# Kernel tuning notes

Hardware: AMD Instinct MI355X
Metric: run time of the kernel (lower is better)

Reference implementation:

```python
import jax, jax.numpy as jnp
import numpy as np

B, LQ, LK = 64, 128, 1024
E, H = 768, 6
HD = E // H            # 128
D2 = HD // 2           # 64
LNUM = 2
QD, KD = 768, 768
EPS = 1e-5


def _gn(x, g, b):
    # torch.nn.GroupNorm(H, E) on 2D input [N, E]: normalize per group of HD channels
    N = x.shape[0]
    xg = x.reshape(N, H, HD)
    m = xg.mean(-1, keepdims=True)
    v = xg.var(-1, keepdims=True)
    xn = ((xg - m) / jnp.sqrt(v + EPS)).reshape(N, E)
    return xn * g + b


def _ln(x, g, b):
    m = x.mean(-1, keepdims=True)
    v = x.var(-1, keepdims=True)
    return (x - m) / jnp.sqrt(v + EPS) * g + b


def setup_inputs() -> dict:
    key = jax.random.key(0)
    ks = iter(jax.random.split(key, 64))
    def rn(shape, s=0.02):
        return jax.random.normal(next(ks), shape, dtype=jnp.float32) * s
    L = LNUM
    inp = {}
    inp['q_feat'] = jax.random.normal(next(ks), (B, LQ, QD), dtype=jnp.float32)
    inp['k_feats'] = jax.random.normal(next(ks), (B, LK, KD), dtype=jnp.float32)
    inp['q_mask'] = jnp.ones((B, LQ), jnp.float32)
    inp['k_mask'] = jnp.ones((B, LK), jnp.float32)
    # per-layer projections (stacked along layer axis)
    inp['Wq'] = rn((L, QD, E)); inp['bq'] = jnp.zeros((L, E)); inp['gq_g'] = jnp.ones((L, E)); inp['gq_b'] = jnp.zeros((L, E))
    inp['Wk'] = rn((L, KD, E)); inp['bk'] = jnp.zeros((L, E)); inp['gk_g'] = jnp.ones((L, E)); inp['gk_b'] = jnp.zeros((L, E))
    inp['Wv1'] = rn((L, QD, E)); inp['bv1'] = jnp.zeros((L, E)); inp['g1_g'] = jnp.ones((L, E)); inp['g1_b'] = jnp.zeros((L, E))
    inp['Wv2'] = rn((L, KD, E)); inp['bv2'] = jnp.zeros((L, E)); inp['g2_g'] = jnp.ones((L, E)); inp['g2_b'] = jnp.zeros((L, E))
    # inner Attention net (per layer)
    inp['Wab'] = rn((L, HD, D2)); inp['bab'] = jnp.zeros((L, D2))
    inp['Wal'] = rn((L, D2, 1)); inp['bal'] = jnp.zeros((L, 1))
    inp['Wac'] = rn((L, D2, HD)); inp['bac'] = jnp.zeros((L, HD))
    # bifeat_emb + layer norms (layer_num-1 of them)
    inp['Wbi'] = rn((L - 1, 2 * E, E)); inp['bbi'] = jnp.zeros((L - 1, E))
    inp['lnb_g'] = jnp.ones((L - 1, E)); inp['lnb_b'] = jnp.zeros((L - 1, E))
    # final proj + layernorm
    inp['Wp'] = rn((E * L + QD, E)); inp['bp'] = jnp.zeros((E,))
    inp['ln_g'] = jnp.ones((E,)); inp['ln_b'] = jnp.zeros((E,))
    return inp


def _bilinear_attention(q, k, kmask, p):
    (Wq, bq, gqg, gqb, Wk, bk, gkg, gkb, Wv1, bv1, g1g, g1b,
     Wv2, bv2, g2g, g2b, Wab, bab, Wal, bal, Wac, bac) = p
    Bb = q.shape[0]
    Lk = k.shape[1]
    qp = _gn(jnp.tanh(q @ Wq + bq), gqg, gqb).reshape(Bb, H, HD)      # [B,H,HD]
    v1 = _gn(jnp.tanh(q @ Wv1 + bv1), g1g, g1b).reshape(Bb, H, HD)
    kf = k.reshape(-1, k.shape[-1])
    kp = _gn(jnp.tanh(kf @ Wk + bk), gkg, gkb).reshape(Bb, Lk, H, HD).transpose(0, 2, 1, 3)   # [B,H,Lk,HD]
    v2 = _gn(jnp.tanh(kf @ Wv2 + bv2), g2g, g2b).reshape(Bb, Lk, H, HD).transpose(0, 2, 1, 3)
    att_map = qp[:, :, None, :] * kp                                  # [B,H,Lk,HD] bilinear map
    basic = jax.nn.relu(att_map @ Wab + bab)                          # [B,H,Lk,D2]
    mext = kmask[:, None, :, None]                                    # [B,1,Lk,1]
    pool = (basic * mext).sum(2) / mext.sum(2)                        # masked mean -> [B,H,D2]
    a_s = (basic @ Wal + bal)[..., 0]                                 # [B,H,Lk]
    a_s = jnp.where(kmask[:, None, :] == 0, -1e9, a_s)
    a_s = jax.nn.softmax(a_s, axis=-1)
    a_c = jax.nn.sigmoid(pool @ Wac + bac)                            # [B,H,HD] channel gate
    v2a = jnp.einsum('bhl,bhld->bhd', a_s, v2)
    return (v1 * v2a * a_c).reshape(Bb, E)


def reference(q_feat, k_feats, q_mask, k_mask,
              Wq, bq, gq_g, gq_b, Wk, bk, gk_g, gk_b,
              Wv1, bv1, g1_g, g1_b, Wv2, bv2, g2_g, g2_b,
              Wab, bab, Wal, bal, Wac, bac,
              Wbi, bbi, lnb_g, lnb_b, Wp, bp, ln_g, ln_b):
    qm = q_mask[..., None]
    q = (q_feat * qm).sum(1) / qm.sum(1)                              # masked mean pool -> [B,QD]
    feats = [q]
    k = k_feats
    for i in range(LNUM):
        p = (Wq[i], bq[i], gq_g[i], gq_b[i], Wk[i], bk[i], gk_g[i], gk_b[i],
             Wv1[i], bv1[i], g1_g[i], g1_b[i], Wv2[i], bv2[i], g2_g[i], g2_b[i],
             Wab[i], bab[i], Wal[i], bal[i], Wac[i], bac[i])
        q = _bilinear_attention(q, k, k_mask, p)                      # dropout = identity (eval)
        feats.append(q)
        if i < LNUM - 1:
            cat = jnp.concatenate([jnp.broadcast_to(q[:, None, :], k.shape), k], axis=-1)
            k = _ln(jax.nn.relu(cat @ Wbi[i] + bbi[i]) + k, lnb_g[i], lnb_b[i])
    out = _ln(jnp.concatenate(feats, axis=-1) @ Wp + bp, ln_g, ln_b)
    return out
```

## Files before the change

kernel.cpp:

```cpp
#include <hip/hip_runtime.h>
#include <math.h>

#define DEVI static __device__ __forceinline__

typedef unsigned short u16;
typedef __attribute__((ext_vector_type(8))) short short8;
typedef __attribute__((ext_vector_type(4))) float f32x4;

DEVI float bf2f(u16 u) { union { float f; unsigned int i; } c; c.i = ((unsigned int)u) << 16; return c.f; }
DEVI u16 f2bf(float f) {
  union { float f; unsigned int i; } c; c.f = f;
  unsigned int r = c.i + 0x7FFFu + ((c.i >> 16) & 1u);
  return (u16)(r >> 16);
}

DEVI float ftanh(float x) {
  float e = __expf(2.f * x);
  return 1.f - 2.f * __builtin_amdgcn_rcpf(e + 1.f);
}

DEVI void gld16(const u16* g, u16* l) {
  __builtin_amdgcn_global_load_lds((const __attribute__((address_space(1))) unsigned int*)g,
                                   (__attribute__((address_space(3))) unsigned int*)l, 16, 0, 0);
}

#define BB 64
#define LQN 128
#define LKN 1024
#define EN 768
#define HN 6
#define HDN 128
#define D2N 64
#define EPSV 1e-5f

__global__ __launch_bounds__(256) void transpose_w5(
    const float* __restrict__ Wk, const float* __restrict__ Wv2,
    const float* __restrict__ Wbi, u16* __restrict__ WkvT,
    u16* __restrict__ WbiT) {
  __shared__ float tile[32][33];
  int z = blockIdx.z;
  const float* src;
  u16* dst;
  if (z < 2) { src = Wk + (size_t)z * EN * EN; dst = WkvT + (size_t)z * 1536 * EN; }
  else if (z < 4) { src = Wv2 + (size_t)(z - 2) * EN * EN; dst = WkvT + (size_t)(z - 2) * 1536 * EN + (size_t)EN * EN; }
  else { src = Wbi + (size_t)EN * EN; dst = WbiT; }
  int kb = blockIdx.x * 32, nb = blockIdx.y * 32;
  int tx = threadIdx.x, ty = threadIdx.y;
  for (int j = 0; j < 32; j += 8)
    tile[ty + j][tx] = src[(size_t)(kb + ty + j) * EN + nb + tx];
  __syncthreads();
  for (int j = 0; j < 32; j += 8)
    dst[(size_t)(nb + ty + j) * EN + kb + tx] = f2bf(tile[tx][ty + j]);
}

__global__ __launch_bounds__(256) void transpose_cvt(
    const float* __restrict__ src, u16* __restrict__ dst, int K, int N,
    size_t srcZ, size_t dstZ) {
  __shared__ float tile[32][33];
  src += (size_t)blockIdx.z * srcZ;
  dst += (size_t)blockIdx.z * dstZ;
  int kb = blockIdx.x * 32, nb = blockIdx.y * 32;
  int tx = threadIdx.x, ty = threadIdx.y;
  for (int j = 0; j < 32; j += 8)
    tile[ty + j][tx] = src[(size_t)(kb + ty + j) * N + nb + tx];
  __syncthreads();
  for (int j = 0; j < 32; j += 8)
    dst[(size_t)(nb + ty + j) * K + kb + tx] = f2bf(tile[tx][ty + j]);
}

__global__ void conv_bf16(const float* __restrict__ src, u16* __restrict__ dst, size_t n8) {
  size_t i = (size_t)blockIdx.x * 256 + threadIdx.x;
  if (i >= n8) return;
  float4 a = ((const float4*)src)[2 * i];
  float4 b = ((const float4*)src)[2 * i + 1];
  short8 o;
  o[0] = (short)f2bf(a.x); o[1] = (short)f2bf(a.y); o[2] = (short)f2bf(a.z); o[3] = (short)f2bf(a.w);
  o[4] = (short)f2bf(b.x); o[5] = (short)f2bf(b.y); o[6] = (short)f2bf(b.z); o[7] = (short)f2bf(b.w);
  *(short8*)&dst[i * 8] = o;
}

__global__ __launch_bounds__(768) void poolq_kernel(
    const float* __restrict__ qf, const float* __restrict__ qm,
    float* __restrict__ q_cur, float* __restrict__ feats) {
  int t = threadIdx.x, b = blockIdx.x;
  float s = 0.f, ms = 0.f;
  for (int l = 0; l < LQN; ++l) {
    float w = qm[b * LQN + l];
    s += qf[((size_t)b * LQN + l) * EN + t] * w;
    ms += w;
  }
  float q = s / ms;
  q_cur[(size_t)b * EN + t] = q;
  feats[(size_t)b * 3 * EN + t] = q;
}

__global__ __launch_bounds__(256) void msum_kernel(const float* __restrict__ km, float* __restrict__ msum) {
  __shared__ float red[256];
  int t = threadIdx.x, b = blockIdx.x;
  float s = 0.f;
  for (int l = t; l < LKN; l += 256) s += km[b * LKN + l];
  red[t] = s; __syncthreads();
  for (int o = 128; o > 0; o >>= 1) { if (t < o) red[t] += red[t + o]; __syncthreads(); }
  if (t == 0) msum[b] = red[0];
}

__global__ __launch_bounds__(768) void qside2_kernel(
    const float* __restrict__ q_in,
    const float* __restrict__ W0, const float* __restrict__ b0,
    const float* __restrict__ g0, const float* __restrict__ bb0, float* __restrict__ o0,
    const float* __restrict__ W1, const float* __restrict__ b1,
    const float* __restrict__ g1, const float* __restrict__ bb1, float* __restrict__ o1,
    const float* __restrict__ W2, const float* __restrict__ b2, float* __restrict__ o2) {
  __shared__ float qs[EN];
  __shared__ float ys[EN];
  __shared__ float mh[HN], rh[HN];
  int t = threadIdx.x, b = blockIdx.x, which = blockIdx.y;
  const float* W = which == 0 ? W0 : (which == 1 ? W1 : W2);
  const float* bvec = which == 0 ? b0 : (which == 1 ? b1 : b2);
  qs[t] = q_in[(size_t)b * EN + t];
  __syncthreads();
  float acc = 0.f;
  for (int k = 0; k < EN; ++k) acc += qs[k] * W[(size_t)k * EN + t];
  if (which == 2) {
    o2[(size_t)b * EN + t] = acc + bvec[t];
    return;
  }
  const float* g = which ? g1 : g0;
  const float* bb = which ? bb1 : bb0;
  float* outp = which ? o1 : o0;
  float y = tanhf(acc + bvec[t]);
  ys[t] = y; __syncthreads();
  if (t < HN) {
    float s = 0.f, s2 = 0.f;
    for (int d = 0; d < HDN; ++d) { float v = ys[t * HDN + d]; s += v; s2 += v * v; }
    float m = s * (1.f / HDN), var = s2 * (1.f / HDN) - m * m;
    mh[t] = m; rh[t] = rsqrtf(var + EPSV);
  }
  __syncthreads();
  int h = t >> 7;
  outp[(size_t)b * EN + t] = (y - mh[h]) * rh[h] * g[t] + bb[t];
}

__global__ __launch_bounds__(256, 4) void gemm_proj(
    const u16* __restrict__ A, const u16* __restrict__ BT,
    const float* __restrict__ bias_k, const float* __restrict__ g_k,
    const float* __restrict__ bb_k, const float* __restrict__ qp,
    const float* __restrict__ bias_v, const float* __restrict__ g_v,
    const float* __restrict__ bb_v, u16* __restrict__ out_v,
    const u16* __restrict__ Wab_g, const float* __restrict__ bab_g,
    const float* __restrict__ Wal_g, const float* __restrict__ bal_g,
    const float* __restrict__ kmask, float* __restrict__ s_out,
    float* __restrict__ pool_part) {
  const int K = EN;
  __shared__ __align__(16) u16 SM[16384];
  __shared__ float part2[128][2][2];
  __shared__ float pool_sh[4][64];
  u16* As = SM;
  u16* Bs = SM + 8192;
  int t = threadIdx.x;
  int w = t >> 6, lane = t & 63;
  int wm = w >> 1, wn = w & 1;

  int bid = blockIdx.x;
  int swz = ((bid & 7) * 768) + (bid >> 3);
  int rowT = swz / 12, cT = swz % 12;
  int rowBase = rowT << 7;

  int koff = (((lane & 3) ^ ((lane >> 3) & 3)) << 3);
  const u16* gA = A + (size_t)(rowBase + (w << 5) + (lane >> 2)) * K + koff;
  const u16* gB = BT + (size_t)((cT << 7) + (w << 5) + (lane >> 2)) * K + koff;

  int lrow = lane & 15, kq = lane >> 4;
  int sOff = ((kq ^ ((lrow >> 1) & 3)) << 3);
  f32x4 acc[4][4] = {};

  u16* lA0b = As + (w << 10);
  u16* lB0b = Bs + (w << 10);
  u16* lA1b = As + 4096 + (w << 10);
  u16* lB1b = Bs + 4096 + (w << 10);

#define PROJ_PREF(LA, LB, k0) \
    { gld16(gA + (k0), LA); gld16(gA + (size_t)16 * K + (k0), LA + 512); \
      gld16(gB + (k0), LB); gld16(gB + (size_t)16 * K + (k0), LB + 512); }

#define PROJ_STEP(BASE) \
    { short8 af[4], bf[4]; \
      _Pragma("unroll") \
      for (int m = 0; m < 4; ++m) \
        af[m] = *(const short8*)&As[(BASE) + ((wm * 64 + m * 16 + lrow) << 5) + sOff]; \
      _Pragma("unroll") \
      for (int n = 0; n < 4; ++n) \
        bf[n] = *(const short8*)&Bs[(BASE) + ((wn * 64 + n * 16 + lrow) << 5) + sOff]; \
      _Pragma("unroll") \
      for (int m = 0; m < 4; ++m) \
        _Pragma("unroll") \
        for (int n = 0; n < 4; ++n) \
          acc[m][n] = __builtin_amdgcn_mfma_f32_16x16x32_bf16(af[m], bf[n], acc[m][n], 0, 0, 0); }

  PROJ_PREF(lA0b, lB0b, 0)
#pragma unroll 1
  for (int p = 0; p < 12; ++p) {
    __syncthreads();
    PROJ_PREF(lA1b, lB1b, (2 * p + 1) << 5)
    PROJ_STEP(0)
    __syncthreads();
    if (p < 11) PROJ_PREF(lA0b, lB0b, (2 * p + 2) << 5)
    PROJ_STEP(4096)
  }
#undef PROJ_PREF
#undef PROJ_STEP

  __syncthreads();

  const int which = cT >= 6;
  const int ecol = ((which ? cT - 6 : cT) << 7);
  const float* bias = which ? bias_v : bias_k;
  const int bidx = rowBase >> 10;

  {
    float biasv[4];
#pragma unroll
    for (int n = 0; n < 4; ++n)
      biasv[n] = bias[ecol + wn * 64 + n * 16 + lrow];
#pragma unroll
    for (int m = 0; m < 4; ++m)
#pragma unroll
      for (int j = 0; j < 4; ++j) {
        int row = wm * 64 + m * 16 + kq * 4 + j;
#pragma unroll
        for (int n = 0; n < 4; ++n) {
          float y = ftanh(acc[m][n][j] + biasv[n]);
          int c = wn * 64 + n * 16 + lrow;
          int sl = c >> 3;
          int so = ((sl & 7) ^ (row & 7)) | (sl & 8);
          SM[row * 128 + (so << 3) + (c & 7)] = f2bf(y);
        }
      }
  }
  __syncthreads();

  {
    int row = t >> 1, ch = t & 1;
    short8 yv8[8];
    float s = 0.f, s2 = 0.f;
#pragma unroll
    for (int s8 = 0; s8 < 8; ++s8) {
      int sl = (ch << 3) + s8;
      int so = ((sl & 7) ^ (row & 7)) | (sl & 8);
      yv8[s8] = *(const short8*)&SM[row * 128 + (so << 3)];
#pragma unroll
      for (int i = 0; i < 8; ++i) {
        float y = bf2f((u16)yv8[s8][i]);
        s += y; s2 += y * y;
      }
    }
    part2[row][ch][0] = s; part2[row][ch][1] = s2;
    __syncthreads();
    float ssum = part2[row][0][0] + part2[row][1][0];
    float q2 = part2[row][0][1] + part2[row][1][1];
    float mean = ssum * (1.f / 128.f);
    float var = q2 * (1.f / 128.f) - mean * mean;
    float rstd = rsqrtf(var + EPSV);
    const float* gp = which ? g_v : g_k;
    const float* bbp = which ? bb_v : bb_k;
    size_t R = (size_t)rowBase + row;
#pragma unroll
    for (int s8 = 0; s8 < 8; ++s8) {
      int sl = (ch << 3) + s8;
      int so = ((sl & 7) ^ (row & 7)) | (sl & 8);
      int e0 = ecol + (sl << 3);
      float4 g0 = *(const float4*)&gp[e0];
      float4 g1 = *(const float4*)&gp[e0 + 4];
      float4 b0 = *(const float4*)&bbp[e0];
      float4 b1 = *(const float4*)&bbp[e0 + 4];
      float gg[8] = {g0.x, g0.y, g0.z, g0.w, g1.x, g1.y, g1.z, g1.w};
      float bv8[8] = {b0.x, b0.y, b0.z, b0.w, b1.x, b1.y, b1.z, b1.w};
      float ov[8];
#pragma unroll
      for (int i = 0; i < 8; ++i)
        ov[i] = (bf2f((u16)yv8[s8][i]) - mean) * rstd * gg[i] + bv8[i];
      if (!which) {
        float4 q0 = *(const float4*)&qp[(size_t)bidx * EN + e0];
        float4 q1 = *(const float4*)&qp[(size_t)bidx * EN + e0 + 4];
        float qq[8] = {q0.x, q0.y, q0.z, q0.w, q1.x, q1.y, q1.z, q1.w};
#pragma unroll
        for (int i = 0; i < 8; ++i) ov[i] *= qq[i];
      }
      short8 o8;
#pragma unroll
      for (int i = 0; i < 8; ++i) o8[i] = (short)f2bf(ov[i]);
      if (which) *(short8*)&out_v[R * EN + e0] = o8;
      else       *(short8*)&SM[row * 128 + (so << 3)] = o8;
    }
  }
  if (which) return;
  __syncthreads();

  const int h = cT;
  const int lt = (rowBase >> 7) & 7;
  f32x4 acc2[2][4] = {};
#pragma unroll
  for (int ks = 0; ks < 4; ++ks) {
    short8 af2[2], bf2[4];
#pragma unroll
    for (int mm = 0; mm < 2; ++mm) {
      int l = w * 32 + mm * 16 + lrow;
      int sl = ks * 4 + kq;
      int so = ((sl & 7) ^ (l & 7)) | (sl & 8);
      af2[mm] = *(const short8*)&SM[l * 128 + so * 8];
    }
#pragma unroll
    for (int n = 0; n < 4; ++n)
      bf2[n] = *(const short8*)&Wab_g[(size_t)(n * 16 + lrow) * 128 + ks * 32 + kq * 8];
#pragma unroll
    for (int mm = 0; mm < 2; ++mm)
#pragma unroll
      for (int n = 0; n < 4; ++n)
        acc2[mm][n] = __builtin_amdgcn_mfma_f32_16x16x32_bf16(af2[mm], bf2[n], acc2[mm][n], 0, 0, 0);
  }

  float wv[4], bv[4];
#pragma unroll
  for (int n = 0; n < 4; ++n) { int c = n * 16 + lrow; wv[n] = Wal_g[c]; bv[n] = bab_g[c]; }
  float kmv[2][4];
  const float* km = kmask + (size_t)bidx * LKN + lt * 128;
#pragma unroll
  for (int mm = 0; mm < 2; ++mm)
#pragma unroll
    for (int j = 0; j < 4; ++j) kmv[mm][j] = km[w * 32 + mm * 16 + kq * 4 + j];
  float balv = bal_g[0];
  float pp[4] = {0.f, 0.f, 0.f, 0.f};
#pragma unroll
  for (int mm = 0; mm < 2; ++mm)
#pragma unroll
    for (int j = 0; j < 4; ++j) {
      float sp = 0.f;
#pragma unroll
      for (int n = 0; n < 4; ++n) {
        float bsv = fmaxf(acc2[mm][n][j] + bv[n], 0.f);
        sp += bsv * wv[n];
        pp[n] += bsv * kmv[mm][j];
      }
      sp += __shfl_xor(sp, 1, 64);
      sp += __shfl_xor(sp, 2, 64);
      sp += __shfl_xor(sp, 4, 64);
      sp += __shfl_xor(sp, 8, 64);
      if (lrow == 0)
        s_out[(((size_t)bidx * HN + h) << 10) + lt * 128 + w * 32 + mm * 16 + kq * 4 + j] = sp + balv;
    }
#pragma unroll
  for (int n = 0; n < 4; ++n) {
    pp[n] += __shfl_xor(pp[n], 16, 64);
    pp[n] += __shfl_xor(pp[n], 32, 64);
  }
  if (lane < 16) {
#pragma unroll
    for (int n = 0; n < 4; ++n) pool_sh[w][n * 16 + lane] = pp[n];
  }
  __syncthreads();
  if (t < 64) {
    float p = pool_sh[0][t] + pool_sh[1][t] + pool_sh[2][t] + pool_sh[3][t];
    pool_part[((((size_t)bidx * HN + h) << 3) + lt) * 64 + t] = p;
  }
}

__global__ __launch_bounds__(256, 4) void gemm_bilin(
    const u16* __restrict__ A, const u16* __restrict__ BT,
    const float* __restrict__ biasB, const u16* __restrict__ resid,
    u16* __restrict__ out) {
  const int K = EN;
  __shared__ __align__(16) u16 SM[16384];
  u16* As = SM;
  u16* Bs = SM + 8192;
  int t = threadIdx.x;
  int w = t >> 6, lane = t & 63;
  int wm = w >> 1, wn = w & 1;

  int bid = blockIdx.x;
  int swz = ((bid & 7) * 384) + (bid >> 3);
  int rowT = swz / 6, cT = swz % 6;
  int rowBase = rowT << 7;
  int colBase = cT << 7;

  int koff = (((lane & 3) ^ ((lane >> 3) & 3)) << 3);
  const u16* gA = A + (size_t)(rowBase + (w << 5) + (lane >> 2)) * K + koff;
  const u16* gB = BT + (size_t)(colBase + (w << 5) + (lane >> 2)) * K + koff;

  int lrow = lane & 15, kq = lane >> 4;
  int sOff = ((kq ^ ((lrow >> 1) & 3)) << 3);
  f32x4 acc[4][4] = {};

  u16* lA0b = As + (w << 10);
  u16* lB0b = Bs + (w << 10);
  u16* lA1b = As + 4096 + (w << 10);
  u16* lB1b = Bs + 4096 + (w << 10);

#define BIL_PREF(LA, LB, k0) \
    { gld16(gA + (k0), LA); gld16(gA + (size_t)16 * K + (k0), LA + 512); \
      gld16(gB + (k0), LB); gld16(gB + (size_t)16 * K + (k0), LB + 512); }

#define BIL_STEP(BASE) \
    { short8 af[4], bf[4]; \
      _Pragma("unroll") \
      for (int m = 0; m < 4; ++m) \
        af[m] = *(const short8*)&As[(BASE) + ((wm * 64 + m * 16 + lrow) << 5) + sOff]; \
      _Pragma("unroll") \
      for (int n = 0; n < 4; ++n) \
        bf[n] = *(const short8*)&Bs[(BASE) + ((wn * 64 + n * 16 + lrow) << 5) + sOff]; \
      _Pragma("unroll") \
      for (int m = 0; m < 4; ++m) \
        _Pragma("unroll") \
        for (int n = 0; n < 4; ++n) \
          acc[m][n] = __builtin_amdgcn_mfma_f32_16x16x32_bf16(af[m], bf[n], acc[m][n], 0, 0, 0); }

  BIL_PREF(lA0b, lB0b, 0)
#pragma unroll 1
  for (int p = 0; p < 12; ++p) {
    __syncthreads();
    BIL_PREF(lA1b, lB1b, (2 * p + 1) << 5)
    BIL_STEP(0)
    __syncthreads();
    if (p < 11) BIL_PREF(lA0b, lB0b, (2 * p + 2) << 5)
    BIL_STEP(4096)
  }
#undef BIL_PREF
#undef BIL_STEP

  __syncthreads();

  const int bidx = rowBase >> 10;
  {
    float qv[4];
#pragma unroll
    for (int n = 0; n < 4; ++n)
      qv[n] = biasB[(size_t)bidx * EN + colBase + wn * 64 + n * 16 + lrow];
#pragma unroll
    for (int m = 0; m < 4; ++m)
#pragma unroll
      for (int j = 0; j < 4; ++j) {
        int row = wm * 64 + m * 16 + kq * 4 + j;
#pragma unroll
        for (int n = 0; n < 4; ++n) {
          float y = fmaxf(acc[m][n][j] + qv[n], 0.f);
          int c = wn * 64 + n * 16 + lrow;
          int sl = c >> 3;
          int so = ((sl & 7) ^ (row & 7)) | (sl & 8);
          SM[row * 128 + (so << 3) + (c & 7)] = f2bf(y);
        }
      }
  }
  __syncthreads();

  {
    int row = t >> 1, ch = t & 1;
    size_t R = (size_t)rowBase + row;
#pragma unroll
    for (int s8 = 0; s8 < 8; ++s8) {
      int sl = (ch << 3) + s8;
      int so = ((sl & 7) ^ (row & 7)) | (sl & 8);
      short8 yv = *(const short8*)&SM[row * 128 + (so << 3)];
      int e0 = colBase + (sl << 3);
      short8 rv = *(const short8*)&resid[R * EN + e0];
      short8 o8;
#pragma unroll
      for (int i = 0; i < 8; ++i)
        o8[i] = (short)f2bf(bf2f((u16)yv[i]) + bf2f((u16)rv[i]));
      *(short8*)&out[R * EN + e0] = o8;
    }
  }
}

__global__ __launch_bounds__(256) void attn_fin(
    const float* __restrict__ s_in, const float* __restrict__ kmask,
    const float* __restrict__ msum, const float* __restrict__ pool_part,
    const float* __restrict__ Wac, const float* __restrict__ bac,
    const u16* __restrict__ v2, const float* __restrict__ v1,
    float* __restrict__ q_cur, float* __restrict__ feats, int slot) {
  __shared__ float as_sh[LKN];
  __shared__ float red[256];
  __shared__ float red8[16][129];
  __shared__ float pool_sh[64];
  __shared__ float ac_sh[128];
  int t = threadIdx.x;
  int h = blockIdx.x, b = blockIdx.y;
  const float* sb = s_in + (((size_t)b * HN + h) << 10);
  const float* km = kmask + (size_t)b * LKN;
  float v[4];
  float mx = -1e30f;
#pragma unroll
  for (int j = 0; j < 4; ++j) {
    int l = t * 4 + j;
    float x = sb[l];
    if (km[l] == 0.f) x = -1e9f;
    v[j] = x; mx = fmaxf(mx, x);
  }
  red[t] = mx; __syncthreads();
  for (int o = 128; o > 0; o >>= 1) { if (t < o) red[t] = fmaxf(red[t], red[t + o]); __syncthreads(); }
  float mxv = red[0];
  __syncthreads();
  float sum = 0.f;
#pragma unroll
  for (int j = 0; j < 4; ++j) { v[j] = __expf(v[j] - mxv); sum += v[j]; }
  red[t] = sum; __syncthreads();
  for (int o = 128; o > 0; o >>= 1) { if (t < o) red[t] += red[t + o]; __syncthreads(); }
  float inv = 1.f / red[0];
#pragma unroll
  for (int j = 0; j < 4; ++j) as_sh[t * 4 + j] = v[j] * inv;
  if (t < 64) {
    float p = 0.f;
    for (int lt = 0; lt < 8; ++lt)
      p += pool_part[((((size_t)b * HN + h) << 3) + lt) * 64 + t];
    pool_sh[t] = p / msum[b];
  }
  __syncthreads();
  if (t < 128) {
    float a = 0.f;
    for (int j = 0; j < 64; ++j) a += pool_sh[j] * Wac[j * HDN + t];
    ac_sh[t] = 1.f / (1.f + __expf(-(a + bac[t])));
  }
  __syncthreads();
  {
    int o = t & 15, sl = t >> 4;
    const u16* vb = v2 + ((size_t)b * LKN) * EN + h * HDN + o * 8;
    float a8[8] = {};
    for (int l = sl; l < LKN; l += 16) {
      short8 u = *(const short8*)&vb[(size_t)l * EN];
      float wgt = as_sh[l];
#pragma unroll
      for (int i = 0; i < 8; ++i) a8[i] += wgt * bf2f((u16)u[i]);
    }
#pragma unroll
    for (int i = 0; i < 8; ++i) red8[sl][o * 8 + i] = a8[i];
  }
  __syncthreads();
  if (t < 128) {
    float va = 0.f;
#pragma unroll
    for (int s = 0; s < 16; ++s) va += red8[s][t];
    size_t idx = (size_t)b * EN + h * HDN + t;
    float q = v1[idx] * va * ac_sh[t];
    q_cur[idx] = q;
    feats[(size_t)b * 3 * EN + slot * EN + h * HDN + t] = q;
  }
}

__global__ __launch_bounds__(256) void ln_rows_kernel(
    const u16* __restrict__ z, const float* __restrict__ g,
    const float* __restrict__ bb, u16* __restrict__ outp) {
  int t = threadIdx.x, w = t >> 6, lane = t & 63;
  size_t R = (size_t)blockIdx.x * 4 + w;
  const u16* zr = z + R * EN;
  float xv[12];
  float s = 0.f, s2 = 0.f;
#pragma unroll
  for (int c = 0; c < 3; ++c) {
    ushort4 u = *(const ushort4*)&zr[c * 256 + lane * 4];
    float v0 = bf2f(u.x), v1 = bf2f(u.y), v2 = bf2f(u.z), v3 = bf2f(u.w);
    xv[c * 4 + 0] = v0; xv[c * 4 + 1] = v1; xv[c * 4 + 2] = v2; xv[c * 4 + 3] = v3;
    s += v0 + v1 + v2 + v3;
    s2 += v0 * v0 + v1 * v1 + v2 * v2 + v3 * v3;
  }
#pragma unroll
  for (int o = 1; o < 64; o <<= 1) { s += __shfl_xor(s, o, 64); s2 += __shfl_xor(s2, o, 64); }
  float m = s * (1.f / EN), var = s2 * (1.f / EN) - m * m;
  float r = rsqrtf(var + EPSV);
#pragma unroll
  for (int c = 0; c < 3; ++c) {
    ushort4 o4;
    int e = c * 256 + lane * 4;
    o4.x = f2bf((xv[c * 4 + 0] - m) * r * g[e + 0] + bb[e + 0]);
    o4.y = f2bf((xv[c * 4 + 1] - m) * r * g[e + 1] + bb[e + 1]);
    o4.z = f2bf((xv[c * 4 + 2] - m) * r * g[e + 2] + bb[e + 2]);
    o4.w = f2bf((xv[c * 4 + 3] - m) * r * g[e + 3] + bb[e + 3]);
    *(ushort4*)&outp[R * EN + e] = o4;
  }
}

__global__ __launch_bounds__(768) void final_kernel(
    const float* __restrict__ feats, const float* __restrict__ Wp,
    const float* __restrict__ bp, const float* __restrict__ g,
    const float* __restrict__ bb, float* __restrict__ outp) {
  __shared__ float fs[2304];
  __shared__ float red[24];
  __shared__ float mv[2];
  int t = threadIdx.x, b = blockIdx.x;
  fs[t] = feats[(size_t)b * 2304 + t];
  fs[t + 768] = feats[(size_t)b * 2304 + 768 + t];
  fs[t + 1536] = feats[(size_t)b * 2304 + 1536 + t];
  __syncthreads();
  float acc = 0.f;
  for (int k = 0; k < 2304; ++k) acc += fs[k] * Wp[(size_t)k * EN + t];
  float y = acc + bp[t];
  float s = y, s2 = y * y;
  for (int o = 32; o > 0; o >>= 1) { s += __shfl_down(s, o, 64); s2 += __shfl_down(s2, o, 64); }
  int wid = t >> 6, lane = t & 63;
  if (lane == 0) { red[wid] = s; red[12 + wid] = s2; }
  __syncthreads();
  if (t == 0) {
    float ts = 0.f, ts2 = 0.f;
    for (int i = 0; i < 12; ++i) { ts += red[i]; ts2 += red[12 + i]; }
    float m = ts * (1.f / EN), var = ts2 * (1.f / EN) - m * m;
    mv[0] = m; mv[1] = rsqrtf(var + EPSV);
  }
  __syncthreads();
  outp[(size_t)b * EN + t] = (y - mv[0]) * mv[1] * g[t] + bb[t];
}

extern "C" void kernel_launch(void* const* d_in, const int* in_sizes, int n_in,
                              void* d_out, int out_size, void* d_ws, size_t ws_size,
                              hipStream_t stream) {
  const float* q_feat = (const float*)d_in[0];
  const float* k_feats = (const float*)d_in[1];
  const float* q_mask = (const float*)d_in[2];
  const float* k_mask = (const float*)d_in[3];
  const float* Wq = (const float*)d_in[4];
  const float* bq = (const float*)d_in[5];
  const float* gq_g = (const float*)d_in[6];
  const float* gq_b = (const float*)d_in[7];
  const float* Wk = (const float*)d_in[8];
  const float* bk = (const float*)d_in[9];
  const float* gk_g = (const float*)d_in[10];
  const float* gk_b = (const float*)d_in[11];
  const float* Wv1 = (const float*)d_in[12];
  const float* bv1 = (const float*)d_in[13];
  const float* g1_g = (const float*)d_in[14];
  const float* g1_b = (const float*)d_in[15];
  const float* Wv2 = (const float*)d_in[16];
  const float* bv2 = (const float*)d_in[17];
  const float* g2_g = (const float*)d_in[18];
  const float* g2_b = (const float*)d_in[19];
  const float* Wab = (const float*)d_in[20];
  const float* bab = (const float*)d_in[21];
  const float* Wal = (const float*)d_in[22];
  const float* bal = (const float*)d_in[23];
  const float* Wac = (const float*)d_in[24];
  const float* bac = (const float*)d_in[25];
  const float* Wbi = (const float*)d_in[26];
  const float* bbi = (const float*)d_in[27];
  const float* lnb_g = (const float*)d_in[28];
  const float* lnb_b = (const float*)d_in[29];
  const float* Wp = (const float*)d_in[30];
  const float* bp = (const float*)d_in[31];
  const float* ln_g = (const float*)d_in[32];
  const float* ln_b = (const float*)d_in[33];
  float* out = (float*)d_out;
  (void)in_sizes; (void)n_in; (void)out_size; (void)ws_size;

  char* ws = (char*)d_ws;
  size_t off = 0;
  auto alloc = [&](size_t bytes) -> char* {
    char* p = ws + off;
    off += (bytes + 255) & ~(size_t)255;
    return p;
  };
  const size_t MK = (size_t)BB * LKN;
  u16* kf = (u16*)alloc(MK * EN * 2);
  u16* zbuf = (u16*)alloc(MK * EN * 2);
  u16* v2b = (u16*)alloc(MK * EN * 2);
  u16* WkvT = (u16*)alloc((size_t)2 * 1536 * EN * 2);
  u16* WbiT = (u16*)alloc((size_t)EN * EN * 2);
  u16* WabT = (u16*)alloc((size_t)2 * D2N * HDN * 2);
  float* feats = (float*)alloc((size_t)BB * 3 * EN * 4);
  float* q_cur = (float*)alloc((size_t)BB * EN * 4);
  float* qp = (float*)alloc((size_t)BB * EN * 4);
  float* v1 = (float*)alloc((size_t)BB * EN * 4);
  float* qpart = (float*)alloc((size_t)BB * EN * 4);
  float* sbuf = (float*)alloc((size_t)BB * HN * LKN * 4);
  float* poolp = (float*)alloc((size_t)BB * HN * 8 * D2N * 4);
  float* msum = (float*)alloc((size_t)BB * 4);

  dim3 tb(32, 8);
  transpose_w5<<<dim3(24, 24, 5), tb, 0, stream>>>(Wk, Wv2, Wbi, WkvT, WbiT);
  transpose_cvt<<<dim3(4, 2, 2), tb, 0, stream>>>(Wab, WabT, HDN, D2N, (size_t)HDN * D2N, (size_t)D2N * HDN);

  conv_bf16<<<24576, 256, 0, stream>>>(k_feats, kf, MK * EN / 8);
  poolq_kernel<<<BB, EN, 0, stream>>>(q_feat, q_mask, q_cur, feats);
  msum_kernel<<<BB, 256, 0, stream>>>(k_mask, msum);

  qside2_kernel<<<dim3(BB, 2), 768, 0, stream>>>(
      q_cur, Wq, bq, gq_g, gq_b, qp,
      Wv1, bv1, g1_g, g1_b, v1, nullptr, nullptr, nullptr);
  gemm_proj<<<6144, 256, 0, stream>>>(
      kf, WkvT, bk, gk_g, gk_b, qp,
      bv2, g2_g, g2_b, v2b,
      WabT, bab, Wal, bal, k_mask, sbuf, poolp);
  attn_fin<<<dim3(HN, BB), 256, 0, stream>>>(
      sbuf, k_mask, msum, poolp, Wac, bac, v2b, v1, q_cur, feats, 1);

  qside2_kernel<<<dim3(BB, 3), 768, 0, stream>>>(
      q_cur, Wq + (size_t)EN * EN, bq + EN, gq_g + EN, gq_b + EN, qp,
      Wv1 + (size_t)EN * EN, bv1 + EN, g1_g + EN, g1_b + EN, v1,
      Wbi, bbi, qpart);
  gemm_bilin<<<3072, 256, 0, stream>>>(kf, WbiT, qpart, kf, zbuf);
  ln_rows_kernel<<<MK / 4, 256, 0, stream>>>(zbuf, lnb_g, lnb_b, kf);
  gemm_proj<<<6144, 256, 0, stream>>>(
      kf, WkvT + (size_t)1536 * EN, bk + EN, gk_g + EN, gk_b + EN, qp,
      bv2 + EN, g2_g + EN, g2_b + EN, v2b,
      WabT + (size_t)D2N * HDN, bab + D2N, Wal + D2N, bal + 1, k_mask, sbuf, poolp);
  attn_fin<<<dim3(HN, BB), 256, 0, stream>>>(
      sbuf, k_mask, msum, poolp, Wac + (size_t)D2N * HDN, bac + HDN, v2b, v1, q_cur, feats, 2);

  final_kernel<<<BB, EN, 0, stream>>>(feats, Wp, bp, ln_g, ln_b, out);
}
```

Before: 971.7 us.

## Fold layer-norm into the next projection GEMM via row stats and weight scaling

The separate LayerNorm pass over the 64K x 768 intermediate is removed. Per-row partial sums are accumulated in the bilinear GEMM epilogue, finished by a small stats kernel, and the LN gain is folded into the layer-2 K/V2 weights. The mean and bias terms are applied as a rank-1 correction (rstd*acc - m*rstd*u + vb) in the projection epilogue. This saves a full read and write of the large activation, at the cost of feeding the GEMM unnormalized bf16 inputs, which can lose precision when row means are large.

```diff
diff --git a/kernel.cpp b/kernel.cpp
--- a/kernel.cpp
+++ b/kernel.cpp
@@ -35,19 +35,23 @@
 
 __global__ __launch_bounds__(256) void transpose_w5(
     const float* __restrict__ Wk, const float* __restrict__ Wv2,
-    const float* __restrict__ Wbi, u16* __restrict__ WkvT,
-    u16* __restrict__ WbiT) {
+    const float* __restrict__ Wbi, const float* __restrict__ lnb_g,
+    u16* __restrict__ WkvT, u16* __restrict__ WbiT) {
   __shared__ float tile[32][33];
   int z = blockIdx.z;
   const float* src;
   u16* dst;
+  bool fold = (z == 1) || (z == 3);
   if (z < 2) { src = Wk + (size_t)z * EN * EN; dst = WkvT + (size_t)z * 1536 * EN; }
   else if (z < 4) { src = Wv2 + (size_t)(z - 2) * EN * EN; dst = WkvT + (size_t)(z - 2) * 1536 * EN + (size_t)EN * EN; }
   else { src = Wbi + (size_t)EN * EN; dst = WbiT; }
   int kb = blockIdx.x * 32, nb = blockIdx.y * 32;
   int tx = threadIdx.x, ty = threadIdx.y;
-  for (int j = 0; j < 32; j += 8)
-    tile[ty + j][tx] = src[(size_t)(kb + ty + j) * EN + nb + tx];
+  for (int j = 0; j < 32; j += 8) {
+    float v = src[(size_t)(kb + ty + j) * EN + nb + tx];
+    if (fold) v *= lnb_g[kb + ty + j];
+    tile[ty + j][tx] = v;
+  }
   __syncthreads();
   for (int j = 0; j < 32; j += 8)
     dst[(size_t)(nb + ty + j) * EN + kb + tx] = f2bf(tile[tx][ty + j]);
@@ -66,6 +70,41 @@
   __syncthreads();
   for (int j = 0; j < 32; j += 8)
     dst[(size_t)(nb + ty + j) * K + kb + tx] = f2bf(tile[tx][ty + j]);
+}
+
+__global__ __launch_bounds__(256) void uv_kernel(
+    const float* __restrict__ WkL1, const float* __restrict__ Wv2L1,
+    const float* __restrict__ g, const float* __restrict__ bbv,
+    const float* __restrict__ bkL1, const float* __restrict__ bv2L1,
+    float* __restrict__ uvec, float* __restrict__ vbvec) {
+  int c = blockIdx.x * 256 + threadIdx.x;
+  int part = c >= EN;
+  int cc = part ? c - EN : c;
+  const float* W = part ? Wv2L1 : WkL1;
+  float u = 0.f, vb = 0.f;
+  for (int k = 0; k < EN; ++k) {
+    float w = W[(size_t)k * EN + cc];
+    u += g[k] * w;
+    vb += bbv[k] * w;
+  }
+  vb += part ? bv2L1[cc] : bkL1[cc];
+  uvec[c] = u;
+  vbvec[c] = vb;
+}
+
+__global__ __launch_bounds__(256) void finstat_kernel(
+    const float2* __restrict__ rowpart, float2* __restrict__ rowstat) {
+  int R = blockIdx.x * 256 + threadIdx.x;
+  float s = 0.f, s2 = 0.f;
+#pragma unroll
+  for (int i = 0; i < 6; ++i) {
+    float2 p = rowpart[(size_t)i * (BB * LKN) + R];
+    s += p.x; s2 += p.y;
+  }
+  float m = s * (1.f / EN);
+  float var = s2 * (1.f / EN) - m * m;
+  float rstd = rsqrtf(var + EPSV);
+  rowstat[R] = make_float2(rstd, -m * rstd);
 }
 
 __global__ void conv_bf16(const float* __restrict__ src, u16* __restrict__ dst, size_t n8) {
@@ -150,7 +189,9 @@
     const u16* __restrict__ Wab_g, const float* __restrict__ bab_g,
     const float* __restrict__ Wal_g, const float* __restrict__ bal_g,
     const float* __restrict__ kmask, float* __restrict__ s_out,
-    float* __restrict__ pool_part) {
+    float* __restrict__ pool_part,
+    const float2* __restrict__ rowstat, const float* __restrict__ uvec,
+    const float* __restrict__ vbvec) {
   const int K = EN;
   __shared__ __align__(16) u16 SM[16384];
   __shared__ float part2[128][2][2];
@@ -218,18 +259,33 @@
   const int bidx = rowBase >> 10;
 
   {
-    float biasv[4];
-#pragma unroll
-    for (int n = 0; n < 4; ++n)
-      biasv[n] = bias[ecol + wn * 64 + n * 16 + lrow];
+    float biasv[4], un[4], vbn[4];
+    if (rowstat) {
+#pragma unroll
+      for (int n = 0; n < 4; ++n) {
+        int cc = (cT << 7) + wn * 64 + n * 16 + lrow;
+        un[n] = uvec[cc]; vbn[n] = vbvec[cc];
+      }
+    } else {
+#pragma unroll
+      for (int n = 0; n < 4; ++n)
+        biasv[n] = bias[ecol + wn * 64 + n * 16 + lrow];
+    }
 #pragma unroll
     for (int m = 0; m < 4; ++m)
 #pragma unroll
       for (int j = 0; j < 4; ++j) {
         int row = wm * 64 + m * 16 + kq * 4 + j;
+        float rstd = 1.f, m2 = 0.f;
+        if (rowstat) {
+          float2 st = rowstat[rowBase + row];
+          rstd = st.x; m2 = st.y;
+        }
 #pragma unroll
         for (int n = 0; n < 4; ++n) {
-          float y = ftanh(acc[m][n][j] + biasv[n]);
+          float pre = rowstat ? (rstd * acc[m][n][j] + m2 * un[n] + vbn[n])
+                              : (acc[m][n][j] + biasv[n]);
+          float y = ftanh(pre);
           int c = wn * 64 + n * 16 + lrow;
           int sl = c >> 3;
           int so = ((sl & 7) ^ (row & 7)) | (sl & 8);
@@ -367,9 +423,10 @@
 __global__ __launch_bounds__(256, 4) void gemm_bilin(
     const u16* __restrict__ A, const u16* __restrict__ BT,
     const float* __restrict__ biasB, const u16* __restrict__ resid,
-    u16* __restrict__ out) {
+    u16* __restrict__ out, float2* __restrict__ rowpart) {
   const int K = EN;
   __shared__ __align__(16) u16 SM[16384];
+  __shared__ float bps[128], bpq[128];
   u16* As = SM;
   u16* Bs = SM + 8192;
   int t = threadIdx.x;
@@ -454,6 +511,7 @@
   {
     int row = t >> 1, ch = t & 1;
     size_t R = (size_t)rowBase + row;
+    float s = 0.f, s2 = 0.f;
 #pragma unroll
     for (int s8 = 0; s8 < 8; ++s8) {
       int sl = (ch << 3) + s8;
@@ -463,10 +521,18 @@
       short8 rv = *(const short8*)&resid[R * EN + e0];
       short8 o8;
 #pragma unroll
-      for (int i = 0; i < 8; ++i)
-        o8[i] = (short)f2bf(bf2f((u16)yv[i]) + bf2f((u16)rv[i]));
+      for (int i = 0; i < 8; ++i) {
+        u16 zb = f2bf(bf2f((u16)yv[i]) + bf2f((u16)rv[i]));
+        o8[i] = (short)zb;
+        float zf = bf2f(zb);
+        s += zf; s2 += zf * zf;
+      }
       *(short8*)&out[R * EN + e0] = o8;
     }
+    if (ch == 1) { bps[row] = s; bpq[row] = s2; }
+    __syncthreads();
+    if (ch == 0)
+      rowpart[(size_t)cT * (BB * LKN) + R] = make_float2(s + bps[row], s2 + bpq[row]);
   }
 }
 
@@ -541,38 +607,6 @@
     float q = v1[idx] * va * ac_sh[t];
     q_cur[idx] = q;
     feats[(size_t)b * 3 * EN + slot * EN + h * HDN + t] = q;
-  }
-}
-
-__global__ __launch_bounds__(256) void ln_rows_kernel(
-    const u16* __restrict__ z, const float* __restrict__ g,
-    const float* __restrict__ bb, u16* __restrict__ outp) {
-  int t = threadIdx.x, w = t >> 6, lane = t & 63;
-  size_t R = (size_t)blockIdx.x * 4 + w;
-  const u16* zr = z + R * EN;
-  float xv[12];
-  float s = 0.f, s2 = 0.f;
-#pragma unroll
-  for (int c = 0; c < 3; ++c) {
-    ushort4 u = *(const ushort4*)&zr[c * 256 + lane * 4];
-    float v0 = bf2f(u.x), v1 = bf2f(u.y), v2 = bf2f(u.z), v3 = bf2f(u.w);
-    xv[c * 4 + 0] = v0; xv[c * 4 + 1] = v1; xv[c * 4 + 2] = v2; xv[c * 4 + 3] = v3;
-    s += v0 + v1 + v2 + v3;
-    s2 += v0 * v0 + v1 * v1 + v2 * v2 + v3 * v3;
-  }
-#pragma unroll
-  for (int o = 1; o < 64; o <<= 1) { s += __shfl_xor(s, o, 64); s2 += __shfl_xor(s2, o, 64); }
-  float m = s * (1.f / EN), var = s2 * (1.f / EN) - m * m;
-  float r = rsqrtf(var + EPSV);
-#pragma unroll
-  for (int c = 0; c < 3; ++c) {
-    ushort4 o4;
-    int e = c * 256 + lane * 4;
-    o4.x = f2bf((xv[c * 4 + 0] - m) * r * g[e + 0] + bb[e + 0]);
-    o4.y = f2bf((xv[c * 4 + 1] - m) * r * g[e + 1] + bb[e + 1]);
-    o4.z = f2bf((xv[c * 4 + 2] - m) * r * g[e + 2] + bb[e + 2]);
-    o4.w = f2bf((xv[c * 4 + 3] - m) * r * g[e + 3] + bb[e + 3]);
-    *(ushort4*)&outp[R * EN + e] = o4;
   }
 }
 
@@ -668,10 +702,16 @@
   float* sbuf = (float*)alloc((size_t)BB * HN * LKN * 4);
   float* poolp = (float*)alloc((size_t)BB * HN * 8 * D2N * 4);
   float* msum = (float*)alloc((size_t)BB * 4);
+  float2* rowpart = (float2*)alloc((size_t)6 * MK * 8);
+  float2* rowstat = (float2*)alloc(MK * 8);
+  float* uvec = (float*)alloc(1536 * 4);
+  float* vbvec = (float*)alloc(1536 * 4);
 
   dim3 tb(32, 8);
-  transpose_w5<<<dim3(24, 24, 5), tb, 0, stream>>>(Wk, Wv2, Wbi, WkvT, WbiT);
+  transpose_w5<<<dim3(24, 24, 5), tb, 0, stream>>>(Wk, Wv2, Wbi, lnb_g, WkvT, WbiT);
   transpose_cvt<<<dim3(4, 2, 2), tb, 0, stream>>>(Wab, WabT, HDN, D2N, (size_t)HDN * D2N, (size_t)D2N * HDN);
+  uv_kernel<<<6, 256, 0, stream>>>(Wk + (size_t)EN * EN, Wv2 + (size_t)EN * EN,
+                                   lnb_g, lnb_b, bk + EN, bv2 + EN, uvec, vbvec);
 
   conv_bf16<<<24576, 256, 0, stream>>>(k_feats, kf, MK * EN / 8);
   poolq_kernel<<<BB, EN, 0, stream>>>(q_feat, q_mask, q_cur, feats);
@@ -683,7 +723,8 @@
   gemm_proj<<<6144, 256, 0, stream>>>(
       kf, WkvT, bk, gk_g, gk_b, qp,
       bv2, g2_g, g2_b, v2b,
-      WabT, bab, Wal, bal, k_mask, sbuf, poolp);
+      WabT, bab, Wal, bal, k_mask, sbuf, poolp,
+      nullptr, nullptr, nullptr);
   attn_fin<<<dim3(HN, BB), 256, 0, stream>>>(
       sbuf, k_mask, msum, poolp, Wac, bac, v2b, v1, q_cur, feats, 1);
 
@@ -691,12 +732,13 @@
       q_cur, Wq + (size_t)EN * EN, bq + EN, gq_g + EN, gq_b + EN, qp,
       Wv1 + (size_t)EN * EN, bv1 + EN, g1_g + EN, g1_b + EN, v1,
       Wbi, bbi, qpart);
-  gemm_bilin<<<3072, 256, 0, stream>>>(kf, WbiT, qpart, kf, zbuf);
-  ln_rows_kernel<<<MK / 4, 256, 0, stream>>>(zbuf, lnb_g, lnb_b, kf);
+  gemm_bilin<<<3072, 256, 0, stream>>>(kf, WbiT, qpart, kf, zbuf, rowpart);
+  finstat_kernel<<<MK / 256, 256, 0, stream>>>(rowpart, rowstat);
   gemm_proj<<<6144, 256, 0, stream>>>(
-      kf, WkvT + (size_t)1536 * EN, bk + EN, gk_g + EN, gk_b + EN, qp,
+      zbuf, WkvT + (size_t)1536 * EN, bk + EN, gk_g + EN, gk_b + EN, qp,
       bv2 + EN, g2_g + EN, g2_b + EN, v2b,
-      WabT + (size_t)D2N * HDN, bab + D2N, Wal + D2N, bal + 1, k_mask, sbuf, poolp);
+      WabT + (size_t)D2N * HDN, bab + D2N, Wal + D2N, bal + 1, k_mask, sbuf, poolp,
+      rowstat, uvec, vbvec);
   attn_fin<<<dim3(HN, BB), 256, 0, stream>>>(
       sbuf, k_mask, msum, poolp, Wac + (size_t)D2N * HDN, bac + HDN, v2b, v1, q_cur, feats, 2);
 
```

Result: slower. 1.006 ms (+3.6%).
